# Performance work log

Hardware: AMD Instinct MI355X
Metric: run time of the kernel (lower is better)

## Reference

```python
import jax, jax.numpy as jnp
import numpy as np

DIM = 512
HID = DIM // 4        # cross-attention inner dim
MLP_HID = int(DIM * 2.0)
EPS = 1e-5


def _xavier(key, shape):
    fan_in, fan_out = shape[0], shape[1]
    limit = float(np.sqrt(6.0 / (fan_in + fan_out)))
    return jax.random.uniform(key, shape, jnp.float32, -limit, limit)


def setup_inputs() -> dict:
    key = jax.random.key(0)
    ks = jax.random.split(key, 12)
    n, v = 8, 2048
    x = jax.random.normal(ks[0], (n, v, DIM), jnp.float32)
    y = jax.random.normal(ks[1], (n, v, DIM), jnp.float32)
    Wq = _xavier(ks[2], (DIM, HID))
    Wk = _xavier(ks[3], (DIM, HID))
    Wv = _xavier(ks[4], (DIM, DIM))
    gamma = jnp.ones((DIM,), jnp.float32)
    beta = jnp.zeros((DIM,), jnp.float32)
    # nn.Linear default init: U(-1/sqrt(fan_in), 1/sqrt(fan_in))
    b1lim = 1.0 / np.sqrt(DIM)
    W1 = jax.random.uniform(ks[5], (DIM, MLP_HID), jnp.float32, -b1lim, b1lim)
    b1 = jax.random.uniform(ks[6], (MLP_HID,), jnp.float32, -b1lim, b1lim)
    b2lim = 1.0 / np.sqrt(MLP_HID)
    W2 = jax.random.uniform(ks[7], (MLP_HID, DIM), jnp.float32, -b2lim, b2lim)
    b2 = jax.random.uniform(ks[8], (DIM,), jnp.float32, -b2lim, b2lim)
    return {"x": x, "y": y, "Wq": Wq, "Wk": Wk, "Wv": Wv,
            "gamma": gamma, "beta": beta, "W1": W1, "b1": b1, "W2": W2, "b2": b2}


def _layernorm(x, gamma, beta):
    mu = jnp.mean(x, axis=-1, keepdims=True)
    var = jnp.var(x, axis=-1, keepdims=True)
    return (x - mu) * jax.lax.rsqrt(var + EPS) * gamma + beta


def reference(x, y, Wq, Wk, Wv, gamma, beta, W1, b1, W2, b2):
    scale = HID ** (-0.5)
    q = jnp.einsum('nvc,co->nvo', x, Wq)          # [n, q, HID]
    k = jnp.einsum('nvc,co->nvo', y, Wk)          # [n, k, HID]
    v = jnp.einsum('nvc,co->nvo', y, Wv)          # [n, k, DIM]
    attn = jax.nn.softmax(jnp.einsum('nqc,nkc->nqk', q, k) * scale, axis=-1)
    x = x + jnp.einsum('nqk,nkc->nqc', attn, v)   # residual + attention
    h = _layernorm(x, gamma, beta)
    h = jax.nn.gelu(h @ W1 + b1, approximate=False) @ W2 + b2
    return x + h
```

## Files before the change

kernel.cpp:

```cpp
#include <hip/hip_runtime.h>
#include <cstddef>
#include <cstdint>

typedef __attribute__((ext_vector_type(8))) short short8;
typedef __attribute__((ext_vector_type(4))) short s16x4;
typedef __attribute__((ext_vector_type(4))) float f32x4;
typedef __attribute__((ext_vector_type(16))) float f32x16;

#define GLOAD_LDS16(gp, lp) __builtin_amdgcn_global_load_lds( \
    (const __attribute__((address_space(1))) void*)(gp),      \
    (__attribute__((address_space(3))) void*)(lp), 16, 0, 0)

__device__ __forceinline__ short f2bf(float f) {
    union { float f; unsigned u; } v; v.f = f;
    unsigned r = v.u + 0x7fffu + ((v.u >> 16) & 1u);
    return (short)(r >> 16);
}

__global__ __launch_bounds__(256) void prep_kernel(
    const float* __restrict__ Wq, const float* __restrict__ Wk,
    const float* __restrict__ Wv, const float* __restrict__ W1,
    const float* __restrict__ W2,
    short* WqT, short* WkT, short* WvT, short* W1T, short* W2T)
{
    __shared__ short tile[64][68];
    int b2 = blockIdx.x;
    const float* in; short* out; int R, C;
    if (b2 < 16)       { in = Wq; out = WqT; R = 512;  C = 128; }
    else if (b2 < 32)  { in = Wk; out = WkT; R = 512;  C = 128;  b2 -= 16; }
    else if (b2 < 96)  { in = Wv; out = WvT; R = 512;  C = 512;  b2 -= 32; }
    else if (b2 < 224) { in = W1; out = W1T; R = 512;  C = 1024; b2 -= 96; }
    else               { in = W2; out = W2T; R = 1024; C = 512;  b2 -= 224; }
    int nx = C >> 6;
    int r0 = (b2 / nx) * 64, c0 = (b2 % nx) * 64;
    int t = threadIdx.x, tr = t >> 6, tc = t & 63;
#pragma unroll
    for (int i = 0; i < 16; ++i) {
        int r = i * 4 + tr;
        tile[r][tc] = f2bf(in[(size_t)(r0 + r) * C + (c0 + tc)]);
    }
    __syncthreads();
#pragma unroll
    for (int i = 0; i < 16; ++i) {
        int r = i * 4 + tr;
        out[(size_t)(c0 + r) * R + (r0 + tc)] = tile[tc][r];
    }
}

__global__ __launch_bounds__(256, 2) void proj_gemm(
    const float* __restrict__ x, const float* __restrict__ y,
    const short* __restrict__ WqT, const short* __restrict__ WkT,
    const short* __restrict__ WvT,
    short* __restrict__ qbf, short* __restrict__ kbff, short* __restrict__ vbf)
{
    __shared__ short As[128][64];
    __shared__ short Bs[128][64];
    int bid = blockIdx.x;
    const float* A; const short* BT; short* outp; int n0, N, mode, mb;
    if (bid < 128)      { A = x; BT = WqT; outp = qbf;  n0 = 0; N = 128; mode = 0; mb = bid; }
    else if (bid < 256) { A = y; BT = WkT; outp = kbff; n0 = 0; N = 128; mode = 0; mb = bid - 128; }
    else { int v2 = bid - 256; A = y; BT = WvT; outp = vbf; n0 = (v2 & 3) << 7; N = 512; mode = 1; mb = v2 >> 2; }
    const int m0 = mb << 7;
    const int K = 512;
    const int t = threadIdx.x, l = t & 63, w = t >> 6;
    const int wm = w >> 1, wn = w & 1;
    const int lo = l & 15, hi = l >> 4;

    f32x4 acc[4][4] = {};
    const int srow = l >> 3;
    const int scg  = (l & 7) ^ (srow & 7);

    for (int kt = 0; kt < K; kt += 64) {
#pragma unroll
        for (int i = 0; i < 4; ++i) {
            int seg = w * 4 + i;
            int row = seg * 8 + srow;
            GLOAD_LDS16(BT + (size_t)(n0 + row) * K + kt + scg * 8, &Bs[seg * 8][0]);
        }
#pragma unroll
        for (int i = 0; i < 4; ++i) {
            int c = i * 256 + t;
            int row = c >> 3, ch = c & 7;
            const float* src = A + (size_t)(m0 + row) * K + kt + ch * 8;
            f32x4 u0 = *(const f32x4*)src;
            f32x4 u1 = *(const f32x4*)(src + 4);
            int d0, d1, d2, d3;
            asm("v_cvt_pk_bf16_f32 %0, %1, %2" : "=v"(d0) : "v"(u0[0]), "v"(u0[1]));
            asm("v_cvt_pk_bf16_f32 %0, %1, %2" : "=v"(d1) : "v"(u0[2]), "v"(u0[3]));
            asm("v_cvt_pk_bf16_f32 %0, %1, %2" : "=v"(d2) : "v"(u1[0]), "v"(u1[1]));
            asm("v_cvt_pk_bf16_f32 %0, %1, %2" : "=v"(d3) : "v"(u1[2]), "v"(u1[3]));
            union { int i[4]; short8 v; } uu;
            uu.i[0] = d0; uu.i[1] = d1; uu.i[2] = d2; uu.i[3] = d3;
            *(short8*)&As[row][((ch ^ (row & 7)) * 8)] = uu.v;
        }
        __syncthreads();
#pragma unroll
        for (int kk = 0; kk < 2; ++kk) {
            short8 af[4], bfv[4];
            const int rc = ((kk * 4 + hi) ^ (lo & 7)) * 8;
#pragma unroll
            for (int mi = 0; mi < 4; ++mi)
                af[mi] = *(const short8*)&As[wm * 64 + mi * 16 + lo][rc];
#pragma unroll
            for (int ni = 0; ni < 4; ++ni)
                bfv[ni] = *(const short8*)&Bs[wn * 64 + ni * 16 + lo][rc];
            __builtin_amdgcn_s_setprio(1);
#pragma unroll
            for (int mi = 0; mi < 4; ++mi)
#pragma unroll
                for (int ni = 0; ni < 4; ++ni)
                    acc[mi][ni] = __builtin_amdgcn_mfma_f32_16x16x32_bf16(
                        af[mi], bfv[ni], acc[mi][ni], 0, 0, 0);
            __builtin_amdgcn_s_setprio(0);
        }
        __syncthreads();
    }

    if (mode == 0) {
#pragma unroll
        for (int mi = 0; mi < 4; ++mi) {
#pragma unroll
            for (int ni = 0; ni < 4; ++ni) {
                int rowb = m0 + wm * 64 + mi * 16 + hi * 4;
                int col  = n0 + wn * 64 + ni * 16 + lo;
                size_t base = ((size_t)(rowb >> 5) * (N >> 4) + (col >> 4)) * 512
                            + ((col & 15) >> 3) * 256 + (rowb & 31) * 8 + (col & 7);
#pragma unroll
                for (int r = 0; r < 4; ++r)
                    outp[base + r * 8] = f2bf(acc[mi][ni][r]);
            }
        }
    } else {
#pragma unroll
        for (int mi = 0; mi < 4; ++mi) {
#pragma unroll
            for (int ni = 0; ni < 4; ++ni) {
                int rowb = m0 + wm * 64 + mi * 16 + hi * 4;
                int col  = n0 + wn * 64 + ni * 16 + lo;
                size_t base = ((size_t)(rowb >> 4) * (N >> 5) + (col >> 5)) * 512
                            + ((rowb & 15) >> 3) * 256 + (col & 31) * 8 + (rowb & 7);
                s16x4 pk;
#pragma unroll
                for (int r = 0; r < 4; ++r) pk[r] = f2bf(acc[mi][ni][r]);
                *(s16x4*)(outp + base) = pk;
            }
        }
    }
}

template<int EPI>
__global__ __launch_bounds__(256, 2) void gemm_kernel(
    const short* __restrict__ A, const short* __restrict__ BT, void* outv,
    const float* __restrict__ bias, const float* __restrict__ resid,
    int N, int K)
{
    __shared__ short As[128][64];
    __shared__ short Bs[128][64];
    int bid = blockIdx.x;
    const int cpx = gridDim.x >> 3;
    bid = (bid & 7) * cpx + (bid >> 3);
    const int nb = N >> 7;
    const int m0 = (bid / nb) << 7;
    const int n0 = (bid % nb) << 7;
    const int t = threadIdx.x, l = t & 63, w = t >> 6;
    const int wm = w >> 1, wn = w & 1;
    const int lo = l & 15, hi = l >> 4;

    f32x4 acc[4][4] = {};
    const int srow = l >> 3;
    const int scg  = (l & 7) ^ (srow & 7);

    for (int kt = 0; kt < K; kt += 64) {
#pragma unroll
        for (int i = 0; i < 4; ++i) {
            int seg = w * 4 + i;
            int row = seg * 8 + srow;
            GLOAD_LDS16(A + (size_t)(m0 + row) * K + kt + scg * 8, &As[seg * 8][0]);
        }
#pragma unroll
        for (int i = 0; i < 4; ++i) {
            int seg = w * 4 + i;
            int row = seg * 8 + srow;
            GLOAD_LDS16(BT + (size_t)(n0 + row) * K + kt + scg * 8, &Bs[seg * 8][0]);
        }
        __syncthreads();
#pragma unroll
        for (int kk = 0; kk < 2; ++kk) {
            short8 af[4], bfv[4];
            const int rc = ((kk * 4 + hi) ^ (lo & 7)) * 8;
#pragma unroll
            for (int mi = 0; mi < 4; ++mi)
                af[mi] = *(const short8*)&As[wm * 64 + mi * 16 + lo][rc];
#pragma unroll
            for (int ni = 0; ni < 4; ++ni)
                bfv[ni] = *(const short8*)&Bs[wn * 64 + ni * 16 + lo][rc];
            __builtin_amdgcn_s_setprio(1);
#pragma unroll
            for (int mi = 0; mi < 4; ++mi)
#pragma unroll
                for (int ni = 0; ni < 4; ++ni)
                    acc[mi][ni] = __builtin_amdgcn_mfma_f32_16x16x32_bf16(
                        af[mi], bfv[ni], acc[mi][ni], 0, 0, 0);
            __builtin_amdgcn_s_setprio(0);
        }
        __syncthreads();
    }

#pragma unroll
    for (int mi = 0; mi < 4; ++mi) {
#pragma unroll
        for (int ni = 0; ni < 4; ++ni) {
#pragma unroll
            for (int r = 0; r < 4; ++r) {
                int row = m0 + wm * 64 + mi * 16 + hi * 4 + r;
                int col = n0 + wn * 64 + ni * 16 + lo;
                size_t idx = (size_t)row * N + col;
                float v = acc[mi][ni][r];
                if (EPI == 2) {
                    v += bias[col];
                    v = 0.5f * v * (1.0f + erff(v * 0.70710678118654752f));
                    ((short*)outv)[idx] = f2bf(v);
                } else {
                    v += bias[col] + resid[idx];
                    ((float*)outv)[idx] = v;
                }
            }
        }
    }
}

__global__ __launch_bounds__(512, 1) void flash_kernel(
    const float* __restrict__ x,
    const short* __restrict__ qbf,
    const short* __restrict__ kbff,
    const short* __restrict__ vbf,
    float* __restrict__ xres,
    const float* __restrict__ gamma,
    const float* __restrict__ beta,
    short* __restrict__ hb)
{
    __shared__ short Ps[2][2][8][512];
    __shared__ float lpart[8][32];
    __shared__ float rsum[8][64];
    __shared__ float rsq[8][64];
    __shared__ float murs[2][64];

    const int bid = blockIdx.x;
    const int n = bid & 7;
    const int qtile = bid >> 3;
    const int q0 = qtile << 6;
    const int t = threadIdx.x, l = t & 63, w = t >> 6;
    const int qh = w >> 2, kq = w & 3;
    const int lo5 = l & 31, hi2 = l >> 5;
    const float C1 = 0.08838834764831845f * 1.4426950408889634f;

    short8 qf[8];
    {
        const short* qp = qbf + (((size_t)(n * 64 + qtile * 2 + qh) * 8) << 9) + l * 8;
#pragma unroll
        for (int s = 0; s < 8; ++s) qf[s] = *(const short8*)(qp + (s << 9));
    }

    f32x16 o00 = {}, o01 = {}, o10 = {}, o11 = {};
    float lp = 0.f;

    const short* kb0 = kbff + (((size_t)(n * 64) * 8) << 9);
    const short* vb0 = vbf + ((((size_t)(n * 128)) * 16 + w * 2) << 9);

    short8 preg0, preg1;

    {
        const short* kp = kb0 + (((size_t)kq * 8) << 9) + l * 8;
        short8 kf[8];
#pragma unroll
        for (int s = 0; s < 8; ++s) kf[s] = *(const short8*)(kp + (s << 9));
        f32x16 sa = {};
        __builtin_amdgcn_s_setprio(1);
#pragma unroll
        for (int s = 0; s < 8; ++s)
            sa = __builtin_amdgcn_mfma_f32_32x32x16_bf16(kf[s], qf[s], sa, 0, 0, 0);
        __builtin_amdgcn_s_setprio(0);
        float lsum = 0.f;
#pragma unroll
        for (int r = 0; r < 16; ++r) {
            float p = exp2f(sa[r] * C1);
            sa[r] = p; lsum += p;
        }
        lp = lsum;
        int wq[8], sx[8];
#pragma unroll
        for (int q2 = 0; q2 < 8; ++q2) {
            int a;
            asm("v_cvt_pk_bf16_f32 %0, %1, %2"
                : "=v"(a) : "v"(sa[2 * q2]), "v"(sa[2 * q2 + 1]));
            wq[q2] = a;
        }
#pragma unroll
        for (int q2 = 0; q2 < 8; ++q2) sx[q2] = __shfl_xor(wq[q2], 32);
        union { int i[4]; short8 v; } u0, u1;
        u0.i[0] = hi2 ? sx[2] : wq[0];
        u0.i[1] = hi2 ? sx[3] : wq[1];
        u0.i[2] = hi2 ? wq[2] : sx[0];
        u0.i[3] = hi2 ? wq[3] : sx[1];
        u1.i[0] = hi2 ? sx[6] : wq[4];
        u1.i[1] = hi2 ? sx[7] : wq[5];
        u1.i[2] = hi2 ? wq[6] : sx[4];
        u1.i[3] = hi2 ? wq[7] : sx[5];
        *(short8*)&Ps[0][qh][kq * 2][l * 8]     = u0.v;
        *(short8*)&Ps[0][qh][kq * 2 + 1][l * 8] = u1.v;
    }

    for (int kt2 = 0; kt2 < 16; ++kt2) {
        const bool hn = kt2 < 15;
        const short* vp = vb0 + (((size_t)(kt2 * 128)) << 9) + l * 8;

        short8 kf[8];
        if (hn) {
            const short* kp = kb0 + (((size_t)((kt2 + 1) * 4 + kq) * 8) << 9) + l * 8;
#pragma unroll
            for (int s = 0; s < 8; ++s) kf[s] = *(const short8*)(kp + (s << 9));
        }
        short8 vfa[8];
#pragma unroll
        for (int p = 0; p < 8; ++p)
            vfa[p] = *(const short8*)(vp + (((size_t)((p >> 1) * 16 + (p & 1))) << 9));

        if (hn) {
            f32x16 sa = {};
            __builtin_amdgcn_s_setprio(1);
#pragma unroll
            for (int s = 0; s < 8; ++s)
                sa = __builtin_amdgcn_mfma_f32_32x32x16_bf16(kf[s], qf[s], sa, 0, 0, 0);
            __builtin_amdgcn_s_setprio(0);
            float lsum = 0.f;
#pragma unroll
            for (int r = 0; r < 16; ++r) {
                float p = exp2f(sa[r] * C1);
                sa[r] = p; lsum += p;
            }
            lp += lsum;
            int wq[8], sx[8];
#pragma unroll
            for (int q2 = 0; q2 < 8; ++q2) {
                int a;
                asm("v_cvt_pk_bf16_f32 %0, %1, %2"
                    : "=v"(a) : "v"(sa[2 * q2]), "v"(sa[2 * q2 + 1]));
                wq[q2] = a;
            }
#pragma unroll
            for (int q2 = 0; q2 < 8; ++q2) sx[q2] = __shfl_xor(wq[q2], 32);
            union { int i[4]; short8 v; } u0, u1;
            u0.i[0] = hi2 ? sx[2] : wq[0];
            u0.i[1] = hi2 ? sx[3] : wq[1];
            u0.i[2] = hi2 ? wq[2] : sx[0];
            u0.i[3] = hi2 ? wq[3] : sx[1];
            u1.i[0] = hi2 ? sx[6] : wq[4];
            u1.i[1] = hi2 ? sx[7] : wq[5];
            u1.i[2] = hi2 ? wq[6] : sx[4];
            u1.i[3] = hi2 ? wq[7] : sx[5];
            preg0 = u0.v; preg1 = u1.v;
        }

        __syncthreads();

        short8 vfb[8];
#pragma unroll
        for (int p = 0; p < 8; ++p)
            vfb[p] = *(const short8*)(vp + (((size_t)((4 + (p >> 1)) * 16 + (p & 1))) << 9));

        if (hn) {
            const int nb2 = (kt2 + 1) & 1;
            *(short8*)&Ps[nb2][qh][kq * 2][l * 8]     = preg0;
            *(short8*)&Ps[nb2][qh][kq * 2 + 1][l * 8] = preg1;
        }

        const int pb = kt2 & 1;
        __builtin_amdgcn_s_setprio(1);
#pragma unroll
        for (int ks = 0; ks < 4; ++ks) {
            short8 p0 = *(const short8*)&Ps[pb][0][ks][l * 8];
            short8 p1 = *(const short8*)&Ps[pb][1][ks][l * 8];
            o00 = __builtin_amdgcn_mfma_f32_32x32x16_bf16(p0, vfa[ks * 2 + 0], o00, 0, 0, 0);
            o01 = __builtin_amdgcn_mfma_f32_32x32x16_bf16(p0, vfa[ks * 2 + 1], o01, 0, 0, 0);
            o10 = __builtin_amdgcn_mfma_f32_32x32x16_bf16(p1, vfa[ks * 2 + 0], o10, 0, 0, 0);
            o11 = __builtin_amdgcn_mfma_f32_32x32x16_bf16(p1, vfa[ks * 2 + 1], o11, 0, 0, 0);
        }
#pragma unroll
        for (int ks = 4; ks < 8; ++ks) {
            short8 p0 = *(const short8*)&Ps[pb][0][ks][l * 8];
            short8 p1 = *(const short8*)&Ps[pb][1][ks][l * 8];
            o00 = __builtin_amdgcn_mfma_f32_32x32x16_bf16(p0, vfb[(ks - 4) * 2 + 0], o00, 0, 0, 0);
            o01 = __builtin_amdgcn_mfma_f32_32x32x16_bf16(p0, vfb[(ks - 4) * 2 + 1], o01, 0, 0, 0);
            o10 = __builtin_amdgcn_mfma_f32_32x32x16_bf16(p1, vfb[(ks - 4) * 2 + 0], o10, 0, 0, 0);
            o11 = __builtin_amdgcn_mfma_f32_32x32x16_bf16(p1, vfb[(ks - 4) * 2 + 1], o11, 0, 0, 0);
        }
        __builtin_amdgcn_s_setprio(0);
    }

    float l2 = lp + __shfl_xor(lp, 32);
    if (l < 32) lpart[w][l] = l2;
    __syncthreads();
    float li0 = 1.f / (lpart[0][lo5] + lpart[1][lo5] + lpart[2][lo5] + lpart[3][lo5]);
    float li1 = 1.f / (lpart[4][lo5] + lpart[5][lo5] + lpart[6][lo5] + lpart[7][lo5]);
    const int c0 = w * 64 + lo5;
#pragma unroll
    for (int r = 0; r < 16; ++r) {
        int qr = (r & 3) + 8 * (r >> 2) + 4 * hi2;
        float ir0 = __shfl(li0, qr);
        float ir1 = __shfl(li1, qr);
        size_t b0 = ((size_t)(n * 2048 + q0 + qr) << 9) + c0;
        size_t b1 = ((size_t)(n * 2048 + q0 + 32 + qr) << 9) + c0;
        float v00 = x[b0]      + o00[r] * ir0;
        float v01 = x[b0 + 32] + o01[r] * ir0;
        float v10 = x[b1]      + o10[r] * ir1;
        float v11 = x[b1 + 32] + o11[r] * ir1;
        xres[b0] = v00; xres[b0 + 32] = v01;
        xres[b1] = v10; xres[b1 + 32] = v11;
        o00[r] = v00; o01[r] = v01; o10[r] = v10; o11[r] = v11;
        float s0 = v00 + v01, sq0 = v00 * v00 + v01 * v01;
        float s1 = v10 + v11, sq1 = v10 * v10 + v11 * v11;
#pragma unroll
        for (int mm = 1; mm < 32; mm <<= 1) {
            s0 += __shfl_xor(s0, mm); sq0 += __shfl_xor(sq0, mm);
            s1 += __shfl_xor(s1, mm); sq1 += __shfl_xor(sq1, mm);
        }
        if (lo5 == 0) {
            rsum[w][qr] = s0;      rsq[w][qr] = sq0;
            rsum[w][32 + qr] = s1; rsq[w][32 + qr] = sq1;
        }
    }
    __syncthreads();
    if (t < 64) {
        float s = 0.f, qq = 0.f;
#pragma unroll
        for (int ww = 0; ww < 8; ++ww) { s += rsum[ww][t]; qq += rsq[ww][t]; }
        float mu = s * (1.0f / 512.0f);
        float var = qq * (1.0f / 512.0f) - mu * mu;
        murs[0][t] = mu;
        murs[1][t] = rsqrtf(var + 1e-5f);
    }
    __syncthreads();
    const float g0 = gamma[c0], g1 = gamma[c0 + 32];
    const float e0 = beta[c0],  e1 = beta[c0 + 32];
#pragma unroll
    for (int r = 0; r < 16; ++r) {
        int qr = (r & 3) + 8 * (r >> 2) + 4 * hi2;
        float mu0 = murs[0][qr],      rs0 = murs[1][qr];
        float mu1 = murs[0][32 + qr], rs1 = murs[1][32 + qr];
        size_t h0 = ((size_t)(n * 2048 + q0 + qr) << 9) + c0;
        size_t h1 = ((size_t)(n * 2048 + q0 + 32 + qr) << 9) + c0;
        hb[h0]      = f2bf((o00[r] - mu0) * rs0 * g0 + e0);
        hb[h0 + 32] = f2bf((o01[r] - mu0) * rs0 * g1 + e1);
        hb[h1]      = f2bf((o10[r] - mu1) * rs1 * g0 + e0);
        hb[h1 + 32] = f2bf((o11[r] - mu1) * rs1 * g1 + e1);
    }
}

extern "C" void kernel_launch(void* const* d_in, const int* in_sizes, int n_in,
                              void* d_out, int out_size, void* d_ws, size_t ws_size,
                              hipStream_t stream)
{
    const float* x     = (const float*)d_in[0];
    const float* y     = (const float*)d_in[1];
    const float* Wq    = (const float*)d_in[2];
    const float* Wk    = (const float*)d_in[3];
    const float* Wv    = (const float*)d_in[4];
    const float* gamma = (const float*)d_in[5];
    const float* beta  = (const float*)d_in[6];
    const float* W1    = (const float*)d_in[7];
    const float* b1    = (const float*)d_in[8];
    const float* W2    = (const float*)d_in[9];
    const float* b2    = (const float*)d_in[10];
    float* out = (float*)d_out;

    char* ws = (char*)d_ws;
    size_t off = 0;
    auto alloc = [&](size_t bytes) -> void* {
        void* p = ws + off;
        off += (bytes + 255) & ~(size_t)255;
        return p;
    };
    short* WqT  = (short*)alloc((size_t)128 * 512 * 2);
    short* WkT  = (short*)alloc((size_t)128 * 512 * 2);
    short* WvT  = (short*)alloc((size_t)512 * 512 * 2);
    short* W1T  = (short*)alloc((size_t)1024 * 512 * 2);
    short* W2T  = (short*)alloc((size_t)512 * 1024 * 2);
    short* qbf  = (short*)alloc((size_t)16384 * 128 * 2);
    short* kbff = (short*)alloc((size_t)16384 * 128 * 2);
    short* vbf  = (short*)alloc((size_t)16384 * 512 * 2);
    short* hb   = (short*)alloc((size_t)16384 * 512 * 2);
    short* gb   = (short*)alloc((size_t)16384 * 1024 * 2);

    prep_kernel<<<352, 256, 0, stream>>>(Wq, Wk, Wv, W1, W2,
                                         WqT, WkT, WvT, W1T, W2T);
    proj_gemm<<<768, 256, 0, stream>>>(x, y, WqT, WkT, WvT, qbf, kbff, vbf);
    flash_kernel<<<256, 512, 0, stream>>>(x, qbf, kbff, vbf, out, gamma, beta, hb);
    gemm_kernel<2><<<1024, 256, 0, stream>>>(hb, W1T, gb, b1, nullptr, 1024, 512);
    gemm_kernel<3><<<512,  256, 0, stream>>>(gb, W2T, out, b2, out, 512, 1024);

    (void)in_sizes; (void)n_in; (void)out_size; (void)ws_size;
}
```

Measured before the change: 168.5 us.

## Split flash attention into 32-query blocks of 4 waves, each computing 128 output columns

The flash kernel changes from 64-query tiles with 8 waves (two query halves by four key quarters) to 32-query tiles with 4 waves, launching 512 blocks of 256 threads with two blocks per CU. Each wave now computes scores for one key quarter and accumulates four 32-column output tiles covering 128 channels. V fragment loads move after the barrier and are issued in two halves of 16. This gives more blocks to fill the CUs and shrinks per-block LDS. In exchange, each wave's output accumulator doubles, raising register pressure, and every K/V tile is reloaded by twice as many blocks.

After: 179.7 us. 6.6% more time.

```diff
diff --git a/kernel.cpp b/kernel.cpp
--- a/kernel.cpp
+++ b/kernel.cpp
@@ -229,7 +229,7 @@
     }
 }
 
-__global__ __launch_bounds__(512, 1) void flash_kernel(
+__global__ __launch_bounds__(256, 2) void flash_kernel(
     const float* __restrict__ x,
     const short* __restrict__ qbf,
     const short* __restrict__ kbff,
@@ -239,38 +239,37 @@
     const float* __restrict__ beta,
     short* __restrict__ hb)
 {
-    __shared__ short Ps[2][2][8][512];
-    __shared__ float lpart[8][32];
-    __shared__ float rsum[8][64];
-    __shared__ float rsq[8][64];
-    __shared__ float murs[2][64];
+    __shared__ short Ps[2][8][512];
+    __shared__ float lpart[4][32];
+    __shared__ float rsum[4][32];
+    __shared__ float rsq[4][32];
+    __shared__ float murs[2][32];
 
     const int bid = blockIdx.x;
     const int n = bid & 7;
     const int qtile = bid >> 3;
-    const int q0 = qtile << 6;
+    const int q0 = qtile << 5;
     const int t = threadIdx.x, l = t & 63, w = t >> 6;
-    const int qh = w >> 2, kq = w & 3;
     const int lo5 = l & 31, hi2 = l >> 5;
     const float C1 = 0.08838834764831845f * 1.4426950408889634f;
 
     short8 qf[8];
     {
-        const short* qp = qbf + (((size_t)(n * 64 + qtile * 2 + qh) * 8) << 9) + l * 8;
+        const short* qp = qbf + (((size_t)(n * 64 + qtile) * 8) << 9) + l * 8;
 #pragma unroll
         for (int s = 0; s < 8; ++s) qf[s] = *(const short8*)(qp + (s << 9));
     }
 
-    f32x16 o00 = {}, o01 = {}, o10 = {}, o11 = {};
+    f32x16 o[4] = {};
     float lp = 0.f;
 
     const short* kb0 = kbff + (((size_t)(n * 64) * 8) << 9);
-    const short* vb0 = vbf + ((((size_t)(n * 128)) * 16 + w * 2) << 9);
+    const short* vb0 = vbf + (((size_t)(n * 128) * 16 + w * 4) << 9);
 
     short8 preg0, preg1;
 
     {
-        const short* kp = kb0 + (((size_t)kq * 8) << 9) + l * 8;
+        const short* kp = kb0 + (((size_t)w * 8) << 9) + l * 8;
         short8 kf[8];
 #pragma unroll
         for (int s = 0; s < 8; ++s) kf[s] = *(const short8*)(kp + (s << 9));
@@ -306,26 +305,18 @@
         u1.i[1] = hi2 ? sx[7] : wq[5];
         u1.i[2] = hi2 ? wq[6] : sx[4];
         u1.i[3] = hi2 ? wq[7] : sx[5];
-        *(short8*)&Ps[0][qh][kq * 2][l * 8]     = u0.v;
-        *(short8*)&Ps[0][qh][kq * 2 + 1][l * 8] = u1.v;
+        *(short8*)&Ps[0][w * 2][l * 8]     = u0.v;
+        *(short8*)&Ps[0][w * 2 + 1][l * 8] = u1.v;
     }
 
     for (int kt2 = 0; kt2 < 16; ++kt2) {
         const bool hn = kt2 < 15;
-        const short* vp = vb0 + (((size_t)(kt2 * 128)) << 9) + l * 8;
-
-        short8 kf[8];
+
         if (hn) {
-            const short* kp = kb0 + (((size_t)((kt2 + 1) * 4 + kq) * 8) << 9) + l * 8;
+            const short* kp = kb0 + (((size_t)((kt2 + 1) * 4 + w) * 8) << 9) + l * 8;
+            short8 kf[8];
 #pragma unroll
             for (int s = 0; s < 8; ++s) kf[s] = *(const short8*)(kp + (s << 9));
-        }
-        short8 vfa[8];
-#pragma unroll
-        for (int p = 0; p < 8; ++p)
-            vfa[p] = *(const short8*)(vp + (((size_t)((p >> 1) * 16 + (p & 1))) << 9));
-
-        if (hn) {
             f32x16 sa = {};
             __builtin_amdgcn_s_setprio(1);
 #pragma unroll
@@ -363,36 +354,44 @@
 
         __syncthreads();
 
-        short8 vfb[8];
-#pragma unroll
-        for (int p = 0; p < 8; ++p)
-            vfb[p] = *(const short8*)(vp + (((size_t)((4 + (p >> 1)) * 16 + (p & 1))) << 9));
-
         if (hn) {
             const int nb2 = (kt2 + 1) & 1;
-            *(short8*)&Ps[nb2][qh][kq * 2][l * 8]     = preg0;
-            *(short8*)&Ps[nb2][qh][kq * 2 + 1][l * 8] = preg1;
+            *(short8*)&Ps[nb2][w * 2][l * 8]     = preg0;
+            *(short8*)&Ps[nb2][w * 2 + 1][l * 8] = preg1;
         }
 
         const int pb = kt2 & 1;
+        const short* vp = vb0 + (((size_t)(kt2 * 8) * 16) << 9) + l * 8;
+
+        short8 vfa[16];
+#pragma unroll
+        for (int ks = 0; ks < 4; ++ks)
+#pragma unroll
+            for (int b = 0; b < 4; ++b)
+                vfa[ks * 4 + b] = *(const short8*)(vp + (((size_t)(ks * 16 + b)) << 9));
         __builtin_amdgcn_s_setprio(1);
 #pragma unroll
         for (int ks = 0; ks < 4; ++ks) {
-            short8 p0 = *(const short8*)&Ps[pb][0][ks][l * 8];
-            short8 p1 = *(const short8*)&Ps[pb][1][ks][l * 8];
-            o00 = __builtin_amdgcn_mfma_f32_32x32x16_bf16(p0, vfa[ks * 2 + 0], o00, 0, 0, 0);
-            o01 = __builtin_amdgcn_mfma_f32_32x32x16_bf16(p0, vfa[ks * 2 + 1], o01, 0, 0, 0);
-            o10 = __builtin_amdgcn_mfma_f32_32x32x16_bf16(p1, vfa[ks * 2 + 0], o10, 0, 0, 0);
-            o11 = __builtin_amdgcn_mfma_f32_32x32x16_bf16(p1, vfa[ks * 2 + 1], o11, 0, 0, 0);
-        }
+            short8 p = *(const short8*)&Ps[pb][ks][l * 8];
+#pragma unroll
+            for (int b = 0; b < 4; ++b)
+                o[b] = __builtin_amdgcn_mfma_f32_32x32x16_bf16(p, vfa[ks * 4 + b], o[b], 0, 0, 0);
+        }
+        __builtin_amdgcn_s_setprio(0);
+
+        short8 vfb[16];
+#pragma unroll
+        for (int ks = 4; ks < 8; ++ks)
+#pragma unroll
+            for (int b = 0; b < 4; ++b)
+                vfb[(ks - 4) * 4 + b] = *(const short8*)(vp + (((size_t)(ks * 16 + b)) << 9));
+        __builtin_amdgcn_s_setprio(1);
 #pragma unroll
         for (int ks = 4; ks < 8; ++ks) {
-            short8 p0 = *(const short8*)&Ps[pb][0][ks][l * 8];
-            short8 p1 = *(const short8*)&Ps[pb][1][ks][l * 8];
-            o00 = __builtin_amdgcn_mfma_f32_32x32x16_bf16(p0, vfb[(ks - 4) * 2 + 0], o00, 0, 0, 0);
-            o01 = __builtin_amdgcn_mfma_f32_32x32x16_bf16(p0, vfb[(ks - 4) * 2 + 1], o01, 0, 0, 0);
-            o10 = __builtin_amdgcn_mfma_f32_32x32x16_bf16(p1, vfb[(ks - 4) * 2 + 0], o10, 0, 0, 0);
-            o11 = __builtin_amdgcn_mfma_f32_32x32x16_bf16(p1, vfb[(ks - 4) * 2 + 1], o11, 0, 0, 0);
+            short8 p = *(const short8*)&Ps[pb][ks][l * 8];
+#pragma unroll
+            for (int b = 0; b < 4; ++b)
+                o[b] = __builtin_amdgcn_mfma_f32_32x32x16_bf16(p, vfb[(ks - 4) * 4 + b], o[b], 0, 0, 0);
         }
         __builtin_amdgcn_s_setprio(0);
     }
@@ -400,40 +399,32 @@
     float l2 = lp + __shfl_xor(lp, 32);
     if (l < 32) lpart[w][l] = l2;
     __syncthreads();
-    float li0 = 1.f / (lpart[0][lo5] + lpart[1][lo5] + lpart[2][lo5] + lpart[3][lo5]);
-    float li1 = 1.f / (lpart[4][lo5] + lpart[5][lo5] + lpart[6][lo5] + lpart[7][lo5]);
-    const int c0 = w * 64 + lo5;
+    float li = 1.f / (lpart[0][lo5] + lpart[1][lo5] + lpart[2][lo5] + lpart[3][lo5]);
+    const int c0 = w * 128 + lo5;
 #pragma unroll
     for (int r = 0; r < 16; ++r) {
         int qr = (r & 3) + 8 * (r >> 2) + 4 * hi2;
-        float ir0 = __shfl(li0, qr);
-        float ir1 = __shfl(li1, qr);
-        size_t b0 = ((size_t)(n * 2048 + q0 + qr) << 9) + c0;
-        size_t b1 = ((size_t)(n * 2048 + q0 + 32 + qr) << 9) + c0;
-        float v00 = x[b0]      + o00[r] * ir0;
-        float v01 = x[b0 + 32] + o01[r] * ir0;
-        float v10 = x[b1]      + o10[r] * ir1;
-        float v11 = x[b1 + 32] + o11[r] * ir1;
-        xres[b0] = v00; xres[b0 + 32] = v01;
-        xres[b1] = v10; xres[b1 + 32] = v11;
-        o00[r] = v00; o01[r] = v01; o10[r] = v10; o11[r] = v11;
-        float s0 = v00 + v01, sq0 = v00 * v00 + v01 * v01;
-        float s1 = v10 + v11, sq1 = v10 * v10 + v11 * v11;
+        float ir = __shfl(li, qr);
+        size_t base = ((size_t)(n * 2048 + q0 + qr) << 9) + c0;
+        float v0 = x[base]      + o[0][r] * ir;
+        float v1 = x[base + 32] + o[1][r] * ir;
+        float v2 = x[base + 64] + o[2][r] * ir;
+        float v3 = x[base + 96] + o[3][r] * ir;
+        xres[base] = v0; xres[base + 32] = v1;
+        xres[base + 64] = v2; xres[base + 96] = v3;
+        o[0][r] = v0; o[1][r] = v1; o[2][r] = v2; o[3][r] = v3;
+        float s = v0 + v1 + v2 + v3;
+        float sq = v0 * v0 + v1 * v1 + v2 * v2 + v3 * v3;
 #pragma unroll
         for (int mm = 1; mm < 32; mm <<= 1) {
-            s0 += __shfl_xor(s0, mm); sq0 += __shfl_xor(sq0, mm);
-            s1 += __shfl_xor(s1, mm); sq1 += __shfl_xor(sq1, mm);
-        }
-        if (lo5 == 0) {
-            rsum[w][qr] = s0;      rsq[w][qr] = sq0;
-            rsum[w][32 + qr] = s1; rsq[w][32 + qr] = sq1;
-        }
+            s += __shfl_xor(s, mm); sq += __shfl_xor(sq, mm);
+        }
+        if (lo5 == 0) { rsum[w][qr] = s; rsq[w][qr] = sq; }
     }
     __syncthreads();
-    if (t < 64) {
-        float s = 0.f, qq = 0.f;
-#pragma unroll
-        for (int ww = 0; ww < 8; ++ww) { s += rsum[ww][t]; qq += rsq[ww][t]; }
+    if (t < 32) {
+        float s  = rsum[0][t] + rsum[1][t] + rsum[2][t] + rsum[3][t];
+        float qq = rsq[0][t]  + rsq[1][t]  + rsq[2][t]  + rsq[3][t];
         float mu = s * (1.0f / 512.0f);
         float var = qq * (1.0f / 512.0f) - mu * mu;
         murs[0][t] = mu;
@@ -441,18 +432,18 @@
     }
     __syncthreads();
     const float g0 = gamma[c0], g1 = gamma[c0 + 32];
+    const float g2 = gamma[c0 + 64], g3 = gamma[c0 + 96];
     const float e0 = beta[c0],  e1 = beta[c0 + 32];
+    const float e2 = beta[c0 + 64], e3 = beta[c0 + 96];
 #pragma unroll
     for (int r = 0; r < 16; ++r) {
         int qr = (r & 3) + 8 * (r >> 2) + 4 * hi2;
-        float mu0 = murs[0][qr],      rs0 = murs[1][qr];
-        float mu1 = murs[0][32 + qr], rs1 = murs[1][32 + qr];
-        size_t h0 = ((size_t)(n * 2048 + q0 + qr) << 9) + c0;
-        size_t h1 = ((size_t)(n * 2048 + q0 + 32 + qr) << 9) + c0;
-        hb[h0]      = f2bf((o00[r] - mu0) * rs0 * g0 + e0);
-        hb[h0 + 32] = f2bf((o01[r] - mu0) * rs0 * g1 + e1);
-        hb[h1]      = f2bf((o10[r] - mu1) * rs1 * g0 + e0);
-        hb[h1 + 32] = f2bf((o11[r] - mu1) * rs1 * g1 + e1);
+        float mu = murs[0][qr], rs = murs[1][qr];
+        size_t base = ((size_t)(n * 2048 + q0 + qr) << 9) + c0;
+        hb[base]      = f2bf((o[0][r] - mu) * rs * g0 + e0);
+        hb[base + 32] = f2bf((o[1][r] - mu) * rs * g1 + e1);
+        hb[base + 64] = f2bf((o[2][r] - mu) * rs * g2 + e2);
+        hb[base + 96] = f2bf((o[3][r] - mu) * rs * g3 + e3);
     }
 }
 
@@ -494,7 +485,7 @@
     prep_kernel<<<352, 256, 0, stream>>>(Wq, Wk, Wv, W1, W2,
                                          WqT, WkT, WvT, W1T, W2T);
     proj_gemm<<<768, 256, 0, stream>>>(x, y, WqT, WkT, WvT, qbf, kbff, vbf);
-    flash_kernel<<<256, 512, 0, stream>>>(x, qbf, kbff, vbf, out, gamma, beta, hb);
+    flash_kernel<<<512, 256, 0, stream>>>(x, qbf, kbff, vbf, out, gamma, beta, hb);
     gemm_kernel<2><<<1024, 256, 0, stream>>>(hb, W1T, gb, b1, nullptr, 1024, 512);
     gemm_kernel<3><<<512,  256, 0, stream>>>(gb, W2T, out, b2, out, 512, 1024);
 
```

## Fuse LayerNorm MLP into flash attention kernel, keeping activations on-chip

Applied to the files above, without the earlier changes.

The two separate MLP GEMM launches are removed. Each attention block now writes its normalized rows into shared memory and computes GELU(h·W1+b1)·W2+b2 plus the residual in place, reading W1/W2 from a pre-swizzled MFMA fragment layout built by the prep kernel. This removes the global round-trips for h, the 1024-wide GELU intermediate and the residual output. In exchange each block holds 128KB of LDS at one block per CU with only 256 blocks, and every block reads the full W1/W2 from global/L2 without LDS staging.

New measurement: 172.4 us. +2.3%, slower.

```diff
diff --git a/kernel.cpp b/kernel.cpp
--- a/kernel.cpp
+++ b/kernel.cpp
@@ -21,29 +21,50 @@
     const float* __restrict__ Wq, const float* __restrict__ Wk,
     const float* __restrict__ Wv, const float* __restrict__ W1,
     const float* __restrict__ W2,
-    short* WqT, short* WkT, short* WvT, short* W1T, short* W2T)
+    short* WqT, short* WkT, short* WvT, short* W1F, short* W2F)
 {
-    __shared__ short tile[64][68];
-    int b2 = blockIdx.x;
-    const float* in; short* out; int R, C;
-    if (b2 < 16)       { in = Wq; out = WqT; R = 512;  C = 128; }
-    else if (b2 < 32)  { in = Wk; out = WkT; R = 512;  C = 128;  b2 -= 16; }
-    else if (b2 < 96)  { in = Wv; out = WvT; R = 512;  C = 512;  b2 -= 32; }
-    else if (b2 < 224) { in = W1; out = W1T; R = 512;  C = 1024; b2 -= 96; }
-    else               { in = W2; out = W2T; R = 1024; C = 512;  b2 -= 224; }
-    int nx = C >> 6;
-    int r0 = (b2 / nx) * 64, c0 = (b2 % nx) * 64;
-    int t = threadIdx.x, tr = t >> 6, tc = t & 63;
-#pragma unroll
-    for (int i = 0; i < 16; ++i) {
-        int r = i * 4 + tr;
-        tile[r][tc] = f2bf(in[(size_t)(r0 + r) * C + (c0 + tc)]);
-    }
-    __syncthreads();
-#pragma unroll
-    for (int i = 0; i < 16; ++i) {
-        int r = i * 4 + tr;
-        out[(size_t)(c0 + r) * R + (r0 + tc)] = tile[tc][r];
+    int bid = blockIdx.x, t = threadIdx.x;
+    if (bid < 96) {
+        __shared__ short tile[64][68];
+        int b2 = bid;
+        const float* in; short* out; int R, C;
+        if (b2 < 16)      { in = Wq; out = WqT; R = 512; C = 128; }
+        else if (b2 < 32) { in = Wk; out = WkT; R = 512; C = 128; b2 -= 16; }
+        else              { in = Wv; out = WvT; R = 512; C = 512; b2 -= 32; }
+        int nx = C >> 6;
+        int r0 = (b2 / nx) * 64, c0 = (b2 % nx) * 64;
+        int tr = t >> 6, tc = t & 63;
+#pragma unroll
+        for (int i = 0; i < 16; ++i) {
+            int r = i * 4 + tr;
+            tile[r][tc] = f2bf(in[(size_t)(r0 + r) * C + (c0 + tc)]);
+        }
+        __syncthreads();
+#pragma unroll
+        for (int i = 0; i < 16; ++i) {
+            int r = i * 4 + tr;
+            out[(size_t)(c0 + r) * R + (r0 + tc)] = tile[tc][r];
+        }
+    } else if (bid < 352) {
+        int flat = (bid - 96) * 256 + t;
+        int nn = flat & 1023, kg = flat >> 10, k0 = kg * 8;
+        short8 sv;
+#pragma unroll
+        for (int j = 0; j < 8; ++j)
+            sv[j] = f2bf(W1[(size_t)(k0 + j) * 1024 + nn]);
+        size_t base = ((size_t)(nn >> 5) * 32 + (k0 >> 4)) * 512
+                    + ((k0 >> 3) & 1) * 256 + (nn & 31) * 8;
+        *(short8*)(W1F + base) = sv;
+    } else {
+        int flat = (bid - 352) * 256 + t;
+        int c = flat & 511, kg = flat >> 9, k0 = kg * 8;
+        short8 sv;
+#pragma unroll
+        for (int j = 0; j < 8; ++j)
+            sv[j] = f2bf(W2[(size_t)(k0 + j) * 512 + c]);
+        size_t base = ((size_t)(k0 >> 4) * 16 + (c >> 5)) * 512
+                    + ((k0 >> 3) & 1) * 256 + (c & 31) * 8;
+        *(short8*)(W2F + base) = sv;
     }
 }
 
@@ -148,102 +169,29 @@
     }
 }
 
-template<int EPI>
-__global__ __launch_bounds__(256, 2) void gemm_kernel(
-    const short* __restrict__ A, const short* __restrict__ BT, void* outv,
-    const float* __restrict__ bias, const float* __restrict__ resid,
-    int N, int K)
-{
-    __shared__ short As[128][64];
-    __shared__ short Bs[128][64];
-    int bid = blockIdx.x;
-    const int cpx = gridDim.x >> 3;
-    bid = (bid & 7) * cpx + (bid >> 3);
-    const int nb = N >> 7;
-    const int m0 = (bid / nb) << 7;
-    const int n0 = (bid % nb) << 7;
-    const int t = threadIdx.x, l = t & 63, w = t >> 6;
-    const int wm = w >> 1, wn = w & 1;
-    const int lo = l & 15, hi = l >> 4;
-
-    f32x4 acc[4][4] = {};
-    const int srow = l >> 3;
-    const int scg  = (l & 7) ^ (srow & 7);
-
-    for (int kt = 0; kt < K; kt += 64) {
-#pragma unroll
-        for (int i = 0; i < 4; ++i) {
-            int seg = w * 4 + i;
-            int row = seg * 8 + srow;
-            GLOAD_LDS16(A + (size_t)(m0 + row) * K + kt + scg * 8, &As[seg * 8][0]);
-        }
-#pragma unroll
-        for (int i = 0; i < 4; ++i) {
-            int seg = w * 4 + i;
-            int row = seg * 8 + srow;
-            GLOAD_LDS16(BT + (size_t)(n0 + row) * K + kt + scg * 8, &Bs[seg * 8][0]);
-        }
-        __syncthreads();
-#pragma unroll
-        for (int kk = 0; kk < 2; ++kk) {
-            short8 af[4], bfv[4];
-            const int rc = ((kk * 4 + hi) ^ (lo & 7)) * 8;
-#pragma unroll
-            for (int mi = 0; mi < 4; ++mi)
-                af[mi] = *(const short8*)&As[wm * 64 + mi * 16 + lo][rc];
-#pragma unroll
-            for (int ni = 0; ni < 4; ++ni)
-                bfv[ni] = *(const short8*)&Bs[wn * 64 + ni * 16 + lo][rc];
-            __builtin_amdgcn_s_setprio(1);
-#pragma unroll
-            for (int mi = 0; mi < 4; ++mi)
-#pragma unroll
-                for (int ni = 0; ni < 4; ++ni)
-                    acc[mi][ni] = __builtin_amdgcn_mfma_f32_16x16x32_bf16(
-                        af[mi], bfv[ni], acc[mi][ni], 0, 0, 0);
-            __builtin_amdgcn_s_setprio(0);
-        }
-        __syncthreads();
-    }
-
-#pragma unroll
-    for (int mi = 0; mi < 4; ++mi) {
-#pragma unroll
-        for (int ni = 0; ni < 4; ++ni) {
-#pragma unroll
-            for (int r = 0; r < 4; ++r) {
-                int row = m0 + wm * 64 + mi * 16 + hi * 4 + r;
-                int col = n0 + wn * 64 + ni * 16 + lo;
-                size_t idx = (size_t)row * N + col;
-                float v = acc[mi][ni][r];
-                if (EPI == 2) {
-                    v += bias[col];
-                    v = 0.5f * v * (1.0f + erff(v * 0.70710678118654752f));
-                    ((short*)outv)[idx] = f2bf(v);
-                } else {
-                    v += bias[col] + resid[idx];
-                    ((float*)outv)[idx] = v;
-                }
-            }
-        }
-    }
-}
-
-__global__ __launch_bounds__(512, 1) void flash_kernel(
+__global__ __launch_bounds__(512, 1) void fused_kernel(
     const float* __restrict__ x,
     const short* __restrict__ qbf,
     const short* __restrict__ kbff,
     const short* __restrict__ vbf,
-    float* __restrict__ xres,
     const float* __restrict__ gamma,
     const float* __restrict__ beta,
-    short* __restrict__ hb)
+    const short* __restrict__ W1F,
+    const float* __restrict__ b1,
+    const short* __restrict__ W2F,
+    const float* __restrict__ b2,
+    float* __restrict__ out)
 {
-    __shared__ short Ps[2][2][8][512];
+    __shared__ __align__(16) char smemA[65536];
+    __shared__ __align__(16) char smemB[65536];
     __shared__ float lpart[8][32];
     __shared__ float rsum[8][64];
     __shared__ float rsq[8][64];
     __shared__ float murs[2][64];
+
+    short* PsB = (short*)smemA;
+    short* hT  = (short*)smemA;
+    short* gbf = (short*)smemB;
 
     const int bid = blockIdx.x;
     const int n = bid & 7;
@@ -306,8 +254,8 @@
         u1.i[1] = hi2 ? sx[7] : wq[5];
         u1.i[2] = hi2 ? wq[6] : sx[4];
         u1.i[3] = hi2 ? wq[7] : sx[5];
-        *(short8*)&Ps[0][qh][kq * 2][l * 8]     = u0.v;
-        *(short8*)&Ps[0][qh][kq * 2 + 1][l * 8] = u1.v;
+        *(short8*)&PsB[((0 * 2 + qh) * 8 + kq * 2) * 512 + l * 8]     = u0.v;
+        *(short8*)&PsB[((0 * 2 + qh) * 8 + kq * 2 + 1) * 512 + l * 8] = u1.v;
     }
 
     for (int kt2 = 0; kt2 < 16; ++kt2) {
@@ -370,16 +318,16 @@
 
         if (hn) {
             const int nb2 = (kt2 + 1) & 1;
-            *(short8*)&Ps[nb2][qh][kq * 2][l * 8]     = preg0;
-            *(short8*)&Ps[nb2][qh][kq * 2 + 1][l * 8] = preg1;
+            *(short8*)&PsB[((nb2 * 2 + qh) * 8 + kq * 2) * 512 + l * 8]     = preg0;
+            *(short8*)&PsB[((nb2 * 2 + qh) * 8 + kq * 2 + 1) * 512 + l * 8] = preg1;
         }
 
         const int pb = kt2 & 1;
         __builtin_amdgcn_s_setprio(1);
 #pragma unroll
         for (int ks = 0; ks < 4; ++ks) {
-            short8 p0 = *(const short8*)&Ps[pb][0][ks][l * 8];
-            short8 p1 = *(const short8*)&Ps[pb][1][ks][l * 8];
+            short8 p0 = *(const short8*)&PsB[((pb * 2 + 0) * 8 + ks) * 512 + l * 8];
+            short8 p1 = *(const short8*)&PsB[((pb * 2 + 1) * 8 + ks) * 512 + l * 8];
             o00 = __builtin_amdgcn_mfma_f32_32x32x16_bf16(p0, vfa[ks * 2 + 0], o00, 0, 0, 0);
             o01 = __builtin_amdgcn_mfma_f32_32x32x16_bf16(p0, vfa[ks * 2 + 1], o01, 0, 0, 0);
             o10 = __builtin_amdgcn_mfma_f32_32x32x16_bf16(p1, vfa[ks * 2 + 0], o10, 0, 0, 0);
@@ -387,8 +335,8 @@
         }
 #pragma unroll
         for (int ks = 4; ks < 8; ++ks) {
-            short8 p0 = *(const short8*)&Ps[pb][0][ks][l * 8];
-            short8 p1 = *(const short8*)&Ps[pb][1][ks][l * 8];
+            short8 p0 = *(const short8*)&PsB[((pb * 2 + 0) * 8 + ks) * 512 + l * 8];
+            short8 p1 = *(const short8*)&PsB[((pb * 2 + 1) * 8 + ks) * 512 + l * 8];
             o00 = __builtin_amdgcn_mfma_f32_32x32x16_bf16(p0, vfb[(ks - 4) * 2 + 0], o00, 0, 0, 0);
             o01 = __builtin_amdgcn_mfma_f32_32x32x16_bf16(p0, vfb[(ks - 4) * 2 + 1], o01, 0, 0, 0);
             o10 = __builtin_amdgcn_mfma_f32_32x32x16_bf16(p1, vfb[(ks - 4) * 2 + 0], o10, 0, 0, 0);
@@ -409,24 +357,22 @@
         float ir0 = __shfl(li0, qr);
         float ir1 = __shfl(li1, qr);
         size_t b0 = ((size_t)(n * 2048 + q0 + qr) << 9) + c0;
-        size_t b1 = ((size_t)(n * 2048 + q0 + 32 + qr) << 9) + c0;
-        float v00 = x[b0]      + o00[r] * ir0;
-        float v01 = x[b0 + 32] + o01[r] * ir0;
-        float v10 = x[b1]      + o10[r] * ir1;
-        float v11 = x[b1 + 32] + o11[r] * ir1;
-        xres[b0] = v00; xres[b0 + 32] = v01;
-        xres[b1] = v10; xres[b1 + 32] = v11;
+        size_t b1i = ((size_t)(n * 2048 + q0 + 32 + qr) << 9) + c0;
+        float v00 = x[b0]       + o00[r] * ir0;
+        float v01 = x[b0 + 32]  + o01[r] * ir0;
+        float v10 = x[b1i]      + o10[r] * ir1;
+        float v11 = x[b1i + 32] + o11[r] * ir1;
         o00[r] = v00; o01[r] = v01; o10[r] = v10; o11[r] = v11;
-        float s0 = v00 + v01, sq0 = v00 * v00 + v01 * v01;
-        float s1 = v10 + v11, sq1 = v10 * v10 + v11 * v11;
+        float s = v00 + v01, sq = v00 * v00 + v01 * v01;
+        float s1r = v10 + v11, sq1r = v10 * v10 + v11 * v11;
 #pragma unroll
         for (int mm = 1; mm < 32; mm <<= 1) {
-            s0 += __shfl_xor(s0, mm); sq0 += __shfl_xor(sq0, mm);
-            s1 += __shfl_xor(s1, mm); sq1 += __shfl_xor(sq1, mm);
+            s += __shfl_xor(s, mm); sq += __shfl_xor(sq, mm);
+            s1r += __shfl_xor(s1r, mm); sq1r += __shfl_xor(sq1r, mm);
         }
         if (lo5 == 0) {
-            rsum[w][qr] = s0;      rsq[w][qr] = sq0;
-            rsum[w][32 + qr] = s1; rsq[w][32 + qr] = sq1;
+            rsum[w][qr] = s;        rsq[w][qr] = sq;
+            rsum[w][32 + qr] = s1r; rsq[w][32 + qr] = sq1r;
         }
     }
     __syncthreads();
@@ -440,19 +386,112 @@
         murs[1][t] = rsqrtf(var + 1e-5f);
     }
     __syncthreads();
-    const float g0 = gamma[c0], g1 = gamma[c0 + 32];
-    const float e0 = beta[c0],  e1 = beta[c0 + 32];
+
+    {
+        const float g0 = gamma[c0], g1 = gamma[c0 + 32];
+        const float e0 = beta[c0],  e1 = beta[c0 + 32];
+        const int d0 = c0, d1 = c0 + 32;
+#pragma unroll
+        for (int r = 0; r < 16; ++r) {
+            int qr = (r & 3) + 8 * (r >> 2) + 4 * hi2;
+            float mu0 = murs[0][qr],      rs0 = murs[1][qr];
+            float mu1 = murs[0][32 + qr], rs1 = murs[1][32 + qr];
+            int row0 = qr, row1 = 32 + qr;
+            hT[row0 * 512 + (((d0 >> 3) ^ (row0 & 31)) << 3) + (d0 & 7)] =
+                f2bf((o00[r] - mu0) * rs0 * g0 + e0);
+            hT[row0 * 512 + (((d1 >> 3) ^ (row0 & 31)) << 3) + (d1 & 7)] =
+                f2bf((o01[r] - mu0) * rs0 * g1 + e1);
+            hT[row1 * 512 + (((d0 >> 3) ^ (row1 & 31)) << 3) + (d0 & 7)] =
+                f2bf((o10[r] - mu1) * rs1 * g0 + e0);
+            hT[row1 * 512 + (((d1 >> 3) ^ (row1 & 31)) << 3) + (d1 & 7)] =
+                f2bf((o11[r] - mu1) * rs1 * g1 + e1);
+        }
+    }
+    __syncthreads();
+
+    f32x16 a2[2][2] = {};
+#pragma unroll 1
+    for (int half = 0; half < 2; ++half) {
+#pragma unroll
+        for (int hb2 = 0; hb2 < 2; ++hb2) {
+            f32x16 s1[2] = {};
+#pragma unroll 4
+            for (int s = 0; s < 32; ++s) {
+                int row = hb2 * 32 + lo5;
+                int ch = (s * 2 + hi2) ^ (row & 31);
+                short8 hf = *(const short8*)&hT[row * 512 + ch * 8];
+#pragma unroll
+                for (int gb = 0; gb < 2; ++gb) {
+                    int nb = half * 16 + w * 2 + gb;
+                    short8 w1v = *(const short8*)(W1F + (size_t)nb * 16384 + s * 512 + l * 8);
+                    s1[gb] = __builtin_amdgcn_mfma_f32_32x32x16_bf16(w1v, hf, s1[gb], 0, 0, 0);
+                }
+            }
+#pragma unroll
+            for (int gb = 0; gb < 2; ++gb) {
+#pragma unroll
+                for (int r = 0; r < 16; ++r) {
+                    int g = half * 512 + w * 64 + gb * 32 + (r & 3) + 8 * (r >> 2) + 4 * hi2;
+                    float vv = s1[gb][r] + b1[g];
+                    s1[gb][r] = 0.5f * vv * (1.0f + erff(vv * 0.70710678118654752f));
+                }
+            }
+#pragma unroll
+            for (int gb = 0; gb < 2; ++gb) {
+                int wq[8], sx[8];
+#pragma unroll
+                for (int q2 = 0; q2 < 8; ++q2) {
+                    int a;
+                    asm("v_cvt_pk_bf16_f32 %0, %1, %2"
+                        : "=v"(a) : "v"(s1[gb][2 * q2]), "v"(s1[gb][2 * q2 + 1]));
+                    wq[q2] = a;
+                }
+#pragma unroll
+                for (int q2 = 0; q2 < 8; ++q2) sx[q2] = __shfl_xor(wq[q2], 32);
+                union { int i[4]; short8 v; } u0, u1;
+                u0.i[0] = hi2 ? sx[2] : wq[0];
+                u0.i[1] = hi2 ? sx[3] : wq[1];
+                u0.i[2] = hi2 ? wq[2] : sx[0];
+                u0.i[3] = hi2 ? wq[3] : sx[1];
+                u1.i[0] = hi2 ? sx[6] : wq[4];
+                u1.i[1] = hi2 ? sx[7] : wq[5];
+                u1.i[2] = hi2 ? wq[6] : sx[4];
+                u1.i[3] = hi2 ? wq[7] : sx[5];
+                int kk0 = w * 4 + gb * 2;
+                *(short8*)&gbf[(hb2 * 32 + kk0) * 512 + l * 8]       = u0.v;
+                *(short8*)&gbf[(hb2 * 32 + kk0 + 1) * 512 + l * 8]   = u1.v;
+            }
+        }
+        __syncthreads();
+
+        __builtin_amdgcn_s_setprio(1);
+#pragma unroll
+        for (int hb2 = 0; hb2 < 2; ++hb2) {
+#pragma unroll 4
+            for (int kk = 0; kk < 32; ++kk) {
+                short8 p = *(const short8*)&gbf[(hb2 * 32 + kk) * 512 + l * 8];
+                int kkg = half * 32 + kk;
+#pragma unroll
+                for (int cb = 0; cb < 2; ++cb) {
+                    short8 w2v = *(const short8*)(W2F + (size_t)(kkg * 16 + w * 2 + cb) * 512 + l * 8);
+                    a2[hb2][cb] = __builtin_amdgcn_mfma_f32_32x32x16_bf16(p, w2v, a2[hb2][cb], 0, 0, 0);
+                }
+            }
+        }
+        __builtin_amdgcn_s_setprio(0);
+        __syncthreads();
+    }
+
+    const float bb0 = b2[c0], bb1 = b2[c0 + 32];
 #pragma unroll
     for (int r = 0; r < 16; ++r) {
         int qr = (r & 3) + 8 * (r >> 2) + 4 * hi2;
-        float mu0 = murs[0][qr],      rs0 = murs[1][qr];
-        float mu1 = murs[0][32 + qr], rs1 = murs[1][32 + qr];
-        size_t h0 = ((size_t)(n * 2048 + q0 + qr) << 9) + c0;
-        size_t h1 = ((size_t)(n * 2048 + q0 + 32 + qr) << 9) + c0;
-        hb[h0]      = f2bf((o00[r] - mu0) * rs0 * g0 + e0);
-        hb[h0 + 32] = f2bf((o01[r] - mu0) * rs0 * g1 + e1);
-        hb[h1]      = f2bf((o10[r] - mu1) * rs1 * g0 + e0);
-        hb[h1 + 32] = f2bf((o11[r] - mu1) * rs1 * g1 + e1);
+        size_t b0 = ((size_t)(n * 2048 + q0 + qr) << 9) + c0;
+        size_t b1i = ((size_t)(n * 2048 + q0 + 32 + qr) << 9) + c0;
+        out[b0]       = o00[r] + a2[0][0][r] + bb0;
+        out[b0 + 32]  = o01[r] + a2[0][1][r] + bb1;
+        out[b1i]      = o10[r] + a2[1][0][r] + bb0;
+        out[b1i + 32] = o11[r] + a2[1][1][r] + bb1;
     }
 }
 
@@ -483,20 +522,17 @@
     short* WqT  = (short*)alloc((size_t)128 * 512 * 2);
     short* WkT  = (short*)alloc((size_t)128 * 512 * 2);
     short* WvT  = (short*)alloc((size_t)512 * 512 * 2);
-    short* W1T  = (short*)alloc((size_t)1024 * 512 * 2);
-    short* W2T  = (short*)alloc((size_t)512 * 1024 * 2);
+    short* W1F  = (short*)alloc((size_t)1024 * 512 * 2);
+    short* W2F  = (short*)alloc((size_t)1024 * 512 * 2);
     short* qbf  = (short*)alloc((size_t)16384 * 128 * 2);
     short* kbff = (short*)alloc((size_t)16384 * 128 * 2);
     short* vbf  = (short*)alloc((size_t)16384 * 512 * 2);
-    short* hb   = (short*)alloc((size_t)16384 * 512 * 2);
-    short* gb   = (short*)alloc((size_t)16384 * 1024 * 2);
-
-    prep_kernel<<<352, 256, 0, stream>>>(Wq, Wk, Wv, W1, W2,
-                                         WqT, WkT, WvT, W1T, W2T);
+
+    prep_kernel<<<608, 256, 0, stream>>>(Wq, Wk, Wv, W1, W2,
+                                         WqT, WkT, WvT, W1F, W2F);
     proj_gemm<<<768, 256, 0, stream>>>(x, y, WqT, WkT, WvT, qbf, kbff, vbf);
-    flash_kernel<<<256, 512, 0, stream>>>(x, qbf, kbff, vbf, out, gamma, beta, hb);
-    gemm_kernel<2><<<1024, 256, 0, stream>>>(hb, W1T, gb, b1, nullptr, 1024, 512);
-    gemm_kernel<3><<<512,  256, 0, stream>>>(gb, W2T, out, b2, out, 512, 1024);
+    fused_kernel<<<256, 512, 0, stream>>>(x, qbf, kbff, vbf, gamma, beta,
+                                          W1F, b1, W2F, b2, out);
 
     (void)in_sizes; (void)n_in; (void)out_size; (void)ws_size;
 }
```

## Double-buffer LDS tiles in projection and GEMM kernels to overlap loads

Applied to the files above, without the earlier changes.

Both the projection GEMM and the generic GEMM kernel now keep two LDS buffers per operand. The next K-tile is issued into the alternate buffer before MFMA work on the current one, so global loads can overlap compute. This doubles shared memory per block to 64 KB, which may limit occupancy under the launch bound of 2 blocks. In proj_gemm the fp32 A loads and bf16 conversion are synchronous VGPR work, so they only partially overlap with compute.

After: 181.0 us. +7.4%, slower.

```diff
diff --git a/kernel.cpp b/kernel.cpp
--- a/kernel.cpp
+++ b/kernel.cpp
@@ -53,8 +53,8 @@
     const short* __restrict__ WvT,
     short* __restrict__ qbf, short* __restrict__ kbff, short* __restrict__ vbf)
 {
-    __shared__ short As[128][64];
-    __shared__ short Bs[128][64];
+    __shared__ short As[2][128][64];
+    __shared__ short Bs[2][128][64];
     int bid = blockIdx.x;
     const float* A; const short* BT; short* outp; int n0, N, mode, mb;
     if (bid < 128)      { A = x; BT = WqT; outp = qbf;  n0 = 0; N = 128; mode = 0; mb = bid; }
@@ -70,12 +70,12 @@
     const int srow = l >> 3;
     const int scg  = (l & 7) ^ (srow & 7);
 
-    for (int kt = 0; kt < K; kt += 64) {
+    auto STAGE = [&](int buf, int kt) {
 #pragma unroll
         for (int i = 0; i < 4; ++i) {
             int seg = w * 4 + i;
             int row = seg * 8 + srow;
-            GLOAD_LDS16(BT + (size_t)(n0 + row) * K + kt + scg * 8, &Bs[seg * 8][0]);
+            GLOAD_LDS16(BT + (size_t)(n0 + row) * K + kt + scg * 8, &Bs[buf][seg * 8][0]);
         }
 #pragma unroll
         for (int i = 0; i < 4; ++i) {
@@ -91,19 +91,27 @@
             asm("v_cvt_pk_bf16_f32 %0, %1, %2" : "=v"(d3) : "v"(u1[2]), "v"(u1[3]));
             union { int i[4]; short8 v; } uu;
             uu.i[0] = d0; uu.i[1] = d1; uu.i[2] = d2; uu.i[3] = d3;
-            *(short8*)&As[row][((ch ^ (row & 7)) * 8)] = uu.v;
-        }
-        __syncthreads();
+            *(short8*)&As[buf][row][((ch ^ (row & 7)) * 8)] = uu.v;
+        }
+    };
+
+    STAGE(0, 0);
+    __syncthreads();
+
+    const int nIter = K >> 6;
+    for (int it = 0; it < nIter; ++it) {
+        const int buf = it & 1;
+        if (it + 1 < nIter) STAGE(buf ^ 1, (it + 1) << 6);
 #pragma unroll
         for (int kk = 0; kk < 2; ++kk) {
             short8 af[4], bfv[4];
             const int rc = ((kk * 4 + hi) ^ (lo & 7)) * 8;
 #pragma unroll
             for (int mi = 0; mi < 4; ++mi)
-                af[mi] = *(const short8*)&As[wm * 64 + mi * 16 + lo][rc];
+                af[mi] = *(const short8*)&As[buf][wm * 64 + mi * 16 + lo][rc];
 #pragma unroll
             for (int ni = 0; ni < 4; ++ni)
-                bfv[ni] = *(const short8*)&Bs[wn * 64 + ni * 16 + lo][rc];
+                bfv[ni] = *(const short8*)&Bs[buf][wn * 64 + ni * 16 + lo][rc];
             __builtin_amdgcn_s_setprio(1);
 #pragma unroll
             for (int mi = 0; mi < 4; ++mi)
@@ -154,8 +162,8 @@
     const float* __restrict__ bias, const float* __restrict__ resid,
     int N, int K)
 {
-    __shared__ short As[128][64];
-    __shared__ short Bs[128][64];
+    __shared__ short As[2][128][64];
+    __shared__ short Bs[2][128][64];
     int bid = blockIdx.x;
     const int cpx = gridDim.x >> 3;
     bid = (bid & 7) * cpx + (bid >> 3);
@@ -170,30 +178,38 @@
     const int srow = l >> 3;
     const int scg  = (l & 7) ^ (srow & 7);
 
-    for (int kt = 0; kt < K; kt += 64) {
+    auto STAGE = [&](int buf, int kt) {
 #pragma unroll
         for (int i = 0; i < 4; ++i) {
             int seg = w * 4 + i;
             int row = seg * 8 + srow;
-            GLOAD_LDS16(A + (size_t)(m0 + row) * K + kt + scg * 8, &As[seg * 8][0]);
+            GLOAD_LDS16(A + (size_t)(m0 + row) * K + kt + scg * 8, &As[buf][seg * 8][0]);
         }
 #pragma unroll
         for (int i = 0; i < 4; ++i) {
             int seg = w * 4 + i;
             int row = seg * 8 + srow;
-            GLOAD_LDS16(BT + (size_t)(n0 + row) * K + kt + scg * 8, &Bs[seg * 8][0]);
-        }
-        __syncthreads();
+            GLOAD_LDS16(BT + (size_t)(n0 + row) * K + kt + scg * 8, &Bs[buf][seg * 8][0]);
+        }
+    };
+
+    STAGE(0, 0);
+    __syncthreads();
+
+    const int nIter = K >> 6;
+    for (int it = 0; it < nIter; ++it) {
+        const int buf = it & 1;
+        if (it + 1 < nIter) STAGE(buf ^ 1, (it + 1) << 6);
 #pragma unroll
         for (int kk = 0; kk < 2; ++kk) {
             short8 af[4], bfv[4];
             const int rc = ((kk * 4 + hi) ^ (lo & 7)) * 8;
 #pragma unroll
             for (int mi = 0; mi < 4; ++mi)
-                af[mi] = *(const short8*)&As[wm * 64 + mi * 16 + lo][rc];
+                af[mi] = *(const short8*)&As[buf][wm * 64 + mi * 16 + lo][rc];
 #pragma unroll
             for (int ni = 0; ni < 4; ++ni)
-                bfv[ni] = *(const short8*)&Bs[wn * 64 + ni * 16 + lo][rc];
+                bfv[ni] = *(const short8*)&Bs[buf][wn * 64 + ni * 16 + lo][rc];
             __builtin_amdgcn_s_setprio(1);
 #pragma unroll
             for (int mi = 0; mi < 4; ++mi)
```
